# Kernel tuning notes

Hardware: AMD Instinct MI355X
Metric: run time of the kernel (lower is better)

The kernel has to match this reference:

```python
import jax, jax.numpy as jnp
import numpy as np

NH = 16          # num_attention_heads
NOPE = 128       # qk_nope_head_dim
ROPE = 64        # qk_rope_head_dim
QHD = NOPE + ROPE  # q_head_dim = 192
VD = 128         # v_head_dim
QLR = 1536       # q_lora_rank
KVLR = 512       # kv_lora_rank
HID = 2048
B, S = 1, 2048
THETA = 10000.0
EPS = 1e-6


def rms_norm(x, w, eps=EPS):
    xf = x.astype(jnp.float32)
    var = jnp.mean(xf * xf, axis=-1, keepdims=True)
    return (w * (xf * jax.lax.rsqrt(var + eps)).astype(x.dtype))


def _deinterleave(x):
    # view(..., d//2, 2).transpose(-1, -2).reshape(..., d): evens then odds
    return jnp.concatenate([x[..., 0::2], x[..., 1::2]], axis=-1)


def _rotate_half(x):
    h = x.shape[-1] // 2
    return jnp.concatenate([-x[..., h:], x[..., :h]], axis=-1)


def setup_inputs() -> dict:
    key = jax.random.key(0)
    ks = jax.random.split(key, 6)
    s = 0.02
    return {
        'hidden_states': jax.random.normal(ks[0], (B, S, HID), jnp.float32),
        'position_ids': jnp.arange(S, dtype=jnp.int32)[None, :],
        'Wqa': jax.random.normal(ks[1], (HID, QLR), jnp.float32) * s,
        'qa_ln_w': jnp.ones((QLR,), jnp.float32),
        'Wqb': jax.random.normal(ks[2], (QLR, NH * QHD), jnp.float32) * s,
        'Wkva': jax.random.normal(ks[3], (HID, KVLR + ROPE), jnp.float32) * s,
        'kv_ln_w': jnp.ones((KVLR,), jnp.float32),
        'Wkvb': jax.random.normal(ks[4], (KVLR, NH * (NOPE + VD)), jnp.float32) * s,
        'Wo': jax.random.normal(ks[5], (NH * VD, HID), jnp.float32) * s,
    }


def reference(hidden_states, position_ids, Wqa, qa_ln_w, Wqb, Wkva, kv_ln_w, Wkvb, Wo):
    b, s, _ = hidden_states.shape
    # Q path: low-rank down -> RMSNorm -> up
    q = rms_norm(hidden_states @ Wqa, qa_ln_w) @ Wqb
    q = q.reshape(b, s, NH, QHD).transpose(0, 2, 1, 3)          # (b,h,s,192)
    q_nope, q_pe = q[..., :NOPE], q[..., NOPE:]
    # KV path: compressed kv + shared rope key
    ckv = hidden_states @ Wkva                                   # (b,s,576)
    c_kv, k_pe = ckv[..., :KVLR], ckv[..., KVLR:]
    k_pe = k_pe.reshape(b, s, 1, ROPE).transpose(0, 2, 1, 3)     # (b,1,s,64)
    kv = rms_norm(c_kv, kv_ln_w) @ Wkvb
    kv = kv.reshape(b, s, NH, NOPE + VD).transpose(0, 2, 1, 3)   # (b,h,s,256)
    k_nope, v = kv[..., :NOPE], kv[..., NOPE:]
    # partial RoPE on the 64-dim rope slices
    inv_freq = 1.0 / (THETA ** (jnp.arange(0, ROPE, 2, dtype=jnp.float32) / ROPE))
    t = jnp.arange(s, dtype=jnp.float32)
    emb = jnp.concatenate([jnp.outer(t, inv_freq)] * 2, axis=-1)  # (s,64)
    cos = jnp.cos(emb)[position_ids][:, None]                     # (b,1,s,64)
    sin = jnp.sin(emb)[position_ids][:, None]
    q_pe = _deinterleave(q_pe)
    k_pe = _deinterleave(k_pe)
    q_pe = q_pe * cos + _rotate_half(q_pe) * sin
    k_pe = k_pe * cos + _rotate_half(k_pe) * sin
    query = jnp.concatenate([q_nope, q_pe], axis=-1)                       # (b,h,s,192)
    key = jnp.concatenate([k_nope, jnp.broadcast_to(k_pe, (b, NH, s, ROPE))], axis=-1)
    # causal attention, softmax_scale = q_head_dim**-0.5
    scale = QHD ** (-0.5)
    scores = jnp.einsum('bhqd,bhkd->bhqk', query, key) * scale
    mask = jnp.tril(jnp.ones((s, s), dtype=bool))
    scores = jnp.where(mask, scores, jnp.finfo(scores.dtype).min)
    probs = jax.nn.softmax(scores, axis=-1)
    attn = jnp.einsum('bhqk,bhkd->bhqd', probs, v)               # (b,h,s,128)
    out = attn.transpose(0, 2, 1, 3).reshape(b, s, NH * VD) @ Wo  # (b,s,hid)
    return out
```

## Files before the change

kernel.cpp:

```cpp
#include <hip/hip_runtime.h>
#include <hip/hip_bf16.h>

typedef unsigned short u16;
typedef _Float16 h16;
typedef h16 h16x8 __attribute__((ext_vector_type(8)));
typedef h16 h16x4 __attribute__((ext_vector_type(4)));
typedef float f32x4 __attribute__((ext_vector_type(4)));

#define S_LEN 2048
#define QLR   1536
#define KVLR  512
#define NHEAD 16
#define QHD   192
#define QHS   200
#define NOPE  128
#define VDIM  128
#define SCALE 0.07216878364870322f
#define FREQC (-0.4152410118609203f)

__device__ __forceinline__ void gld16(const h16* g, h16* l){
  __builtin_amdgcn_global_load_lds((__attribute__((address_space(1))) const void*)g,
                                   (__attribute__((address_space(3))) void*)l, 16, 0, 0);
}

__global__ __launch_bounds__(256) void k_cvt(const float* __restrict__ in, h16* __restrict__ out, int n4){
  int i = blockIdx.x * 256 + threadIdx.x;
  if (i < n4){
    float4 v = ((const float4*)in)[i];
    h16x4 o = { (h16)v.x, (h16)v.y, (h16)v.z, (h16)v.w };
    ((h16x4*)out)[i] = o;
  }
}

__global__ __launch_bounds__(256) void k_tc(const float* __restrict__ W, h16* __restrict__ WT, int K, int N){
  __shared__ float t[64][65];
  int k0 = blockIdx.y * 64, n0 = blockIdx.x * 64;
  int tid = threadIdx.x;
  int r = tid >> 4, c4 = (tid & 15) * 4;
#pragma unroll
  for (int it = 0; it < 4; it++){
    float4 v = *(const float4*)(W + (size_t)(k0 + it*16 + r) * N + n0 + c4);
    t[it*16+r][c4] = v.x; t[it*16+r][c4+1] = v.y; t[it*16+r][c4+2] = v.z; t[it*16+r][c4+3] = v.w;
  }
  __syncthreads();
  int n = tid >> 2, k16 = (tid & 3) * 16;
  h16x8 o0, o1;
#pragma unroll
  for (int e = 0; e < 8; e++){ o0[e] = (h16)t[k16 + e][n]; o1[e] = (h16)t[k16 + 8 + e][n]; }
  h16* dst = WT + (size_t)(n0 + n) * K + k0 + k16;
  *(h16x8*)dst = o0;
  *(h16x8*)(dst + 8) = o1;
}

__device__ __forceinline__ void gemm_core(const h16* __restrict__ A, const h16* __restrict__ B,
    int K, int m0, int n0, h16* As, h16* Bs, f32x4 (&acc)[4][4]){
  const int tid = threadIdx.x;
  const int lane = tid & 63, quad = lane >> 4, lr = lane & 15;
  const int wid = tid >> 6;
  const int wr = (wid >> 1) * 64, wc = (wid & 1) * 64;
  const int sr = tid >> 2, scc = (tid & 3) * 8;
  const h16* Ag = A + (size_t)(m0 + sr) * K + scc;
  const h16* Bg = B + (size_t)(n0 + sr) * K + scc;
  for (int kt = 0; kt < K; kt += 32){
    gld16(Ag + kt,                 &As[tid * 8]);
    gld16(Ag + (size_t)64*K + kt,  &As[2048 + tid * 8]);
    gld16(Bg + kt,                 &Bs[tid * 8]);
    gld16(Bg + (size_t)64*K + kt,  &Bs[2048 + tid * 8]);
    __syncthreads();
    h16x8 af[4], bfr[4];
#pragma unroll
    for (int r = 0; r < 4; r++) af[r]  = *(const h16x8*)&As[(wr + r*16 + lr) * 32 + quad * 8];
#pragma unroll
    for (int c = 0; c < 4; c++) bfr[c] = *(const h16x8*)&Bs[(wc + c*16 + lr) * 32 + quad * 8];
#pragma unroll
    for (int r = 0; r < 4; r++)
#pragma unroll
      for (int c = 0; c < 4; c++)
        acc[r][c] = __builtin_amdgcn_mfma_f32_16x16x32_f16(af[r], bfr[c], acc[r][c], 0, 0, 0);
    __syncthreads();
  }
}

template<bool OF32>
__global__ __launch_bounds__(256) void k_gemm(const h16* __restrict__ A, const h16* __restrict__ B,
                                              void* __restrict__ Cv, int N, int K){
  __shared__ __attribute__((aligned(16))) h16 As[128*32];
  __shared__ __attribute__((aligned(16))) h16 Bs[128*32];
  const int m0 = blockIdx.y * 128, n0 = blockIdx.x * 128;
  f32x4 acc[4][4] = {};
  gemm_core(A, B, K, m0, n0, As, Bs, acc);
  const int lane = threadIdx.x & 63, quad = lane >> 4, lr = lane & 15;
  const int wid = threadIdx.x >> 6;
  const int wr = (wid >> 1) * 64, wc = (wid & 1) * 64;
#pragma unroll
  for (int r = 0; r < 4; r++)
#pragma unroll
    for (int c = 0; c < 4; c++){
      int row = m0 + wr + r*16 + quad*4;
      int col = n0 + wc + c*16 + lr;
#pragma unroll
      for (int i = 0; i < 4; i++){
        float val = acc[r][c][i];
        if (OF32) ((float*)Cv)[(size_t)(row + i) * N + col] = val;
        else      ((h16*)Cv)[(size_t)(row + i) * N + col] = (h16)val;
      }
    }
}

__global__ __launch_bounds__(256) void k_norm(const h16* __restrict__ Cc,
      const float* __restrict__ qw, const float* __restrict__ kw, const int* __restrict__ pos_ids,
      h16* __restrict__ qln, h16* __restrict__ kvln, h16* __restrict__ kpe,
      float* __restrict__ cst, float* __restrict__ snt){
  const int s = blockIdx.x, tid = threadIdx.x;
  __shared__ float red[8];
  const h16* c1 = Cc + (size_t)s * 2176;
  float v[6]; float ss = 0.f;
#pragma unroll
  for (int i = 0; i < 6; i++){ v[i] = (float)c1[tid + i*256]; ss += v[i]*v[i]; }
  for (int off = 32; off > 0; off >>= 1) ss += __shfl_down(ss, off);
  if ((tid & 63) == 0) red[tid >> 6] = ss;
  __syncthreads();
  float rq = rsqrtf((red[0]+red[1]+red[2]+red[3]) / (float)QLR + 1e-6f);
#pragma unroll
  for (int i = 0; i < 6; i++)
    qln[(size_t)s * QLR + tid + i*256] = (h16)(qw[tid + i*256] * v[i] * rq);

  const h16* ck = c1 + QLR;
  float w0 = (float)ck[tid], w1 = (float)ck[tid + 256];
  float ss2 = w0*w0 + w1*w1;
  for (int off = 32; off > 0; off >>= 1) ss2 += __shfl_down(ss2, off);
  if ((tid & 63) == 0) red[4 + (tid >> 6)] = ss2;
  __syncthreads();
  float rk = rsqrtf((red[4]+red[5]+red[6]+red[7]) / (float)KVLR + 1e-6f);
  kvln[(size_t)s * KVLR + tid]       = (h16)(kw[tid] * w0 * rk);
  kvln[(size_t)s * KVLR + tid + 256] = (h16)(kw[tid + 256] * w1 * rk);

  if (tid < 32){
    int d = tid;
    float x = (float)ck[KVLR + 2*d];
    float y = (float)ck[KVLR + 2*d + 1];
    float a = (float)pos_ids[s] * exp2f(FREQC * (float)d);
    float cs = cosf(a), sn = sinf(a);
    cst[s*32 + d] = cs; snt[s*32 + d] = sn;
    kpe[(size_t)s*64 + d]      = (h16)(x*cs - y*sn);
    kpe[(size_t)s*64 + 32 + d] = (h16)(y*cs + x*sn);
  }
}

__global__ __launch_bounds__(256) void k_asm(const h16* __restrict__ Qm, const h16* __restrict__ KVm,
      const h16* __restrict__ kpe, const float* __restrict__ cst, const float* __restrict__ snt,
      h16* __restrict__ Qh, h16* __restrict__ Kh, h16* __restrict__ VT){
  const int t = blockIdx.x, h = blockIdx.y, tid = threadIdx.x;
  const int s0 = t * 64;
#pragma unroll
  for (int it = 0; it < 6; it++){
    int cid = it*256 + tid;
    int r = cid / 24, c8 = (cid - r*24) * 8;
    int rr = s0 + r;
    const h16* in = Qm + (size_t)rr*3072 + h*192;
    h16* outr = Qh + ((size_t)h*S_LEN + rr)*QHS;
    h16x8 v = *(const h16x8*)(in + c8);
    if (c8 < 128){
      h16x8 o;
#pragma unroll
      for (int e = 0; e < 8; e++) o[e] = (h16)((float)v[e] * SCALE);
      *(h16x8*)(outr + c8) = o;
    } else {
      int k4 = (c8 - 128) >> 1;
      h16x4 xo, yo;
#pragma unroll
      for (int m2 = 0; m2 < 4; m2++){
        float x = (float)v[2*m2], y = (float)v[2*m2+1];
        float cs = cst[rr*32 + k4 + m2], sn = snt[rr*32 + k4 + m2];
        xo[m2] = (h16)((x*cs - y*sn) * SCALE);
        yo[m2] = (h16)((y*cs + x*sn) * SCALE);
      }
      *(h16x4*)(outr + 128 + k4) = xo;
      *(h16x4*)(outr + 160 + k4) = yo;
    }
  }
#pragma unroll
  for (int it = 0; it < 6; it++){
    int cid = it*256 + tid;
    int r = cid / 24, c8 = (cid - r*24) * 8;
    int rr = s0 + r;
    h16* outr = Kh + ((size_t)h*S_LEN + rr)*QHS;
    if (c8 < 128){
      h16x8 v = *(const h16x8*)(KVm + (size_t)rr*4096 + h*256 + c8);
      *(h16x8*)(outr + c8) = v;
    } else {
      h16x8 v = *(const h16x8*)(kpe + (size_t)rr*64 + (c8 - 128));
      *(h16x8*)(outr + c8) = v;
    }
  }
  {
    int dv = tid >> 1, half = tid & 1;
    const h16* vin = KVm + h*256 + 128 + dv;
    h16* vout = VT + ((size_t)(h*VDIM + dv))*S_LEN + s0;
#pragma unroll
    for (int k = 0; k < 4; k++){
      h16x8 o;
#pragma unroll
      for (int e = 0; e < 8; e++)
        o[e] = vin[(size_t)(s0 + half*32 + k*8 + e) * 4096];
      *(h16x8*)(vout + ((half*32 + k*8 + 8*(dv & 7)) & 63)) = o;
    }
  }
}

__global__ __launch_bounds__(256) void k_flash(const h16* __restrict__ Qh, const h16* __restrict__ Kh,
      const h16* __restrict__ VT, h16* __restrict__ Opart, float* __restrict__ ml){
  const int tile = 31 - blockIdx.x;
  const int h = blockIdx.y;
  const int p = blockIdx.z;
  const int jlo = p * 8;
  if (jlo > tile) return;
  const int jhi = min(jlo + 8, tile + 1);
  const int m0 = tile * 64;
  __shared__ __attribute__((aligned(16))) h16 Ksm[64*QHS];
  __shared__ __attribute__((aligned(16))) h16 Vsm[144*64];
  __shared__ __attribute__((aligned(16))) h16 Psm[64*72];
  const int tid = threadIdx.x, wid = tid >> 6, lane = tid & 63, quad = lane >> 4, lr = lane & 15;

  {
    h16x4 one4 = { (h16)1.f, (h16)1.f, (h16)1.f, (h16)1.f };
    *(h16x4*)&Vsm[128*64 + tid*4] = one4;
  }

  const h16* Qg = Qh + ((size_t)h*S_LEN + m0)*QHS;
#pragma unroll
  for (int i = 0; i < 6; i++) gld16(Qg + i*2048 + tid*8, &Ksm[i*2048 + tid*8]);
  if (wid == 0) gld16(Qg + 12288 + lane*8, &Ksm[12288 + lane*8]);
  __syncthreads();
  h16x8 qf[6];
#pragma unroll
  for (int ks = 0; ks < 6; ks++)
    qf[ks] = *(const h16x8*)&Ksm[(wid*16 + lr)*QHS + ks*32 + quad*8];
  __syncthreads();

  float mst[4];
  f32x4 oacc[9] = {};
#pragma unroll
  for (int i = 0; i < 4; i++) mst[i] = -1e30f;

  for (int j = jlo; j < jhi; ++j){
    const h16* Kg = Kh + ((size_t)h*S_LEN + j*64)*QHS;
#pragma unroll
    for (int i = 0; i < 6; i++) gld16(Kg + i*2048 + tid*8, &Ksm[i*2048 + tid*8]);
    if (wid == 0) gld16(Kg + 12288 + lane*8, &Ksm[12288 + lane*8]);
    const h16* Vg = VT + (size_t)h * VDIM * S_LEN + (size_t)j * 64;
#pragma unroll
    for (int i = 0; i < 4; i++)
      gld16(Vg + (size_t)(i*32 + (tid >> 3)) * S_LEN + (tid & 7)*8, &Vsm[i*2048 + tid*8]);
    __syncthreads();

    f32x4 sc[4] = {};
#pragma unroll
    for (int ks = 0; ks < 6; ks++)
#pragma unroll
      for (int ct = 0; ct < 4; ct++){
        h16x8 kf = *(const h16x8*)&Ksm[(ct*16 + lr)*QHS + ks*32 + quad*8];
        sc[ct] = __builtin_amdgcn_mfma_f32_16x16x32_f16(qf[ks], kf, sc[ct], 0,0,0);
      }

    if (j == tile){
#pragma unroll
      for (int ct = 0; ct < 4; ct++)
#pragma unroll
        for (int i = 0; i < 4; i++)
          if (ct*16 + lr > wid*16 + quad*4 + i) sc[ct][i] = -1e30f;
    }

    float al[4];
#pragma unroll
    for (int i = 0; i < 4; i++){
      float m = fmaxf(fmaxf(sc[0][i], sc[1][i]), fmaxf(sc[2][i], sc[3][i]));
#pragma unroll
      for (int off = 1; off < 16; off <<= 1) m = fmaxf(m, __shfl_xor(m, off));
      float mn = fmaxf(mst[i], m);
      al[i] = __expf(mst[i] - mn);
      mst[i] = mn;
    }
#pragma unroll
    for (int ct = 0; ct < 4; ct++)
#pragma unroll
      for (int i = 0; i < 4; i++)
        Psm[(wid*16 + quad*4 + i)*72 + ct*16 + lr] = (h16)__expf(sc[ct][i] - mst[i]);
#pragma unroll
    for (int oc = 0; oc < 9; oc++)
#pragma unroll
      for (int i = 0; i < 4; i++) oacc[oc][i] *= al[i];

#pragma unroll
    for (int ks2 = 0; ks2 < 2; ks2++){
      h16x8 pf = *(const h16x8*)&Psm[(wid*16 + lr)*72 + ks2*32 + quad*8];
#pragma unroll
      for (int oc = 0; oc < 9; oc++){
        int cv = (ks2*32 + quad*8 + 8*(lr & 7)) & 63;
        h16x8 vf = *(const h16x8*)&Vsm[(oc*16 + lr)*64 + cv];
        oacc[oc] = __builtin_amdgcn_mfma_f32_16x16x32_f16(pf, vf, oacc[oc], 0,0,0);
      }
    }
    __syncthreads();
  }

  const int part = (tile*NHEAD + h)*4 + p;
  h16* Op = Opart + (size_t)part * 8192;
#pragma unroll
  for (int oc = 0; oc < 8; oc++)
#pragma unroll
    for (int i = 0; i < 4; i++)
      Op[(wid*16 + quad*4 + i)*128 + oc*16 + lr] = (h16)oacc[oc][i];
  if (lr == 0){
#pragma unroll
    for (int i = 0; i < 4; i++){
      int r = wid*16 + quad*4 + i;
      ml[(size_t)part*128 + r*2]     = mst[i];
      ml[(size_t)part*128 + r*2 + 1] = oacc[8][i];
    }
  }
}

__global__ __launch_bounds__(256) void k_comb(const h16* __restrict__ Opart, const float* __restrict__ ml,
                                              h16* __restrict__ Ob){
  const int t = blockIdx.x, h = blockIdx.y, tid = threadIdx.x;
  const int P = t/8 + 1;
  const int r = tid >> 2, c0 = (tid & 3) * 32;
  const int base = (t*NHEAD + h)*4;
  float w[4]; float M = -1e30f, denom = 0.f;
  for (int p = 0; p < P; p++) M = fmaxf(M, ml[(size_t)(base+p)*128 + r*2]);
  for (int p = 0; p < P; p++){
    w[p] = __expf(ml[(size_t)(base+p)*128 + r*2] - M);
    denom += w[p] * ml[(size_t)(base+p)*128 + r*2 + 1];
  }
  float inv = 1.f / denom;
#pragma unroll
  for (int ch = 0; ch < 4; ch++){
    float a[8] = {};
    for (int p = 0; p < P; p++){
      h16x8 v = *(const h16x8*)&Opart[(size_t)(base+p)*8192 + r*128 + c0 + ch*8];
#pragma unroll
      for (int e = 0; e < 8; e++) a[e] += w[p] * (float)v[e];
    }
    h16x8 o;
#pragma unroll
    for (int e = 0; e < 8; e++) o[e] = (h16)(a[e] * inv);
    *(h16x8*)&Ob[((size_t)(t*64 + r))*(NHEAD*VDIM) + h*VDIM + c0 + ch*8] = o;
  }
}

extern "C" void kernel_launch(void* const* d_in, const int* in_sizes, int n_in,
                              void* d_out, int out_size, void* d_ws, size_t ws_size,
                              hipStream_t stream){
  const float* hidden = (const float*)d_in[0];
  const int*   pos    = (const int*)  d_in[1];
  const float* Wqa    = (const float*)d_in[2];
  const float* qaw    = (const float*)d_in[3];
  const float* Wqb    = (const float*)d_in[4];
  const float* Wkva   = (const float*)d_in[5];
  const float* kvw    = (const float*)d_in[6];
  const float* Wkvb   = (const float*)d_in[7];
  const float* Wo     = (const float*)d_in[8];

  h16* ws = (h16*)d_ws;
  size_t off = 0;
  auto take = [&](size_t n){ h16* p = ws + off; off += n; return p; };
  h16* hb    = take(2048ull * 2048);
  h16* Wc    = take(2176ull * 2048);
  h16* WqbT  = take(3072ull * 1536);
  h16* WkvbT = take(4096ull * 512);
  h16* WoT   = take(2048ull * 2048);
  h16* Ccomb = take(2048ull * 2176);
  h16* qln   = take(2048ull * 1536);
  h16* kvln  = take(2048ull * 512);
  h16* kpe   = take(2048ull * 64);
  float* cst = (float*)take(2048ull * 64);
  float* snt = (float*)take(2048ull * 64);
  h16* Qm    = take(2048ull * 3072);
  h16* KVm   = take(2048ull * 4096);
  h16* Qh    = take(16ull * 2048 * QHS);
  h16* Kh    = take(16ull * 2048 * QHS);
  h16* VT    = take(16ull * 128 * 2048);
  h16* Ob    = hb;
  h16*   Opart = qln;
  float* mlbuf = (float*)Wc;

  k_cvt<<<4096, 256, 0, stream>>>(hidden, hb, 1048576);
  k_tc<<<dim3(24, 32), 256, 0, stream>>>(Wqa,  Wc,                 2048, 1536);
  k_tc<<<dim3( 9, 32), 256, 0, stream>>>(Wkva, Wc + 1536ull*2048,  2048, 576);
  k_tc<<<dim3(48, 24), 256, 0, stream>>>(Wqb,  WqbT,  1536, 3072);
  k_tc<<<dim3(64,  8), 256, 0, stream>>>(Wkvb, WkvbT, 512,  4096);
  k_tc<<<dim3(32, 32), 256, 0, stream>>>(Wo,   WoT,   2048, 2048);

  k_gemm<false><<<dim3(17, 16), 256, 0, stream>>>(hb, Wc, Ccomb, 2176, 2048);
  k_norm<<<2048, 256, 0, stream>>>(Ccomb, qaw, kvw, pos, qln, kvln, kpe, cst, snt);
  k_gemm<false><<<dim3(24, 16), 256, 0, stream>>>(qln,  WqbT,  Qm,  3072, 1536);
  k_gemm<false><<<dim3(32, 16), 256, 0, stream>>>(kvln, WkvbT, KVm, 4096, 512);
  k_asm<<<dim3(32, 16), 256, 0, stream>>>(Qm, KVm, kpe, cst, snt, Qh, Kh, VT);
  k_flash<<<dim3(32, 16, 4), 256, 0, stream>>>(Qh, Kh, VT, Opart, mlbuf);
  k_comb<<<dim3(32, 16), 256, 0, stream>>>(Opart, mlbuf, Ob);
  k_gemm<true><<<dim3(16, 16), 256, 0, stream>>>(Ob, WoT, d_out, 2048, 2048);
}
```

Baseline: 398.6 us.

## Fuse head assembly into Q/KV GEMM epilogues and double flash query tile

Removes the separate k_asm pass. Q-up GEMM now writes scaled, RoPE-rotated Q straight into the per-head padded layout, KV-up GEMM writes K-nope and transposed V (via an LDS transpose), and k_norm broadcasts the rotated k_pe into Kh. This drops the Qm/KVm intermediates and an extra read-write pass over them. The flash kernel now processes 128 query rows per block (two 16-row tiles per wave, sharing each K/V tile load), with k_comb adjusted to match. The cost is strided scalar epilogue stores, more registers in flash, and fewer flash blocks.

```diff
diff --git a/kernel.cpp b/kernel.cpp
--- a/kernel.cpp
+++ b/kernel.cpp
@@ -13,7 +13,6 @@
 #define NHEAD 16
 #define QHD   192
 #define QHS   200
-#define NOPE  128
 #define VDIM  128
 #define SCALE 0.07216878364870322f
 #define FREQC (-0.4152410118609203f)
@@ -107,12 +106,101 @@
     }
 }
 
+__global__ __launch_bounds__(256) void k_gemm_q(const h16* __restrict__ A, const h16* __restrict__ B,
+      h16* __restrict__ Qh, const float* __restrict__ cst, const float* __restrict__ snt){
+  __shared__ __attribute__((aligned(16))) h16 As[128*32];
+  __shared__ __attribute__((aligned(16))) h16 Bs[128*32];
+  const int m0 = blockIdx.y * 128, n0 = blockIdx.x * 128;
+  f32x4 acc[4][4] = {};
+  gemm_core(A, B, QLR, m0, n0, As, Bs, acc);
+  const int lane = threadIdx.x & 63, quad = lane >> 4, lr = lane & 15;
+  const int wid = threadIdx.x >> 6;
+  const int wr = (wid >> 1) * 64, wc = (wid & 1) * 64;
+#pragma unroll
+  for (int r = 0; r < 4; r++)
+#pragma unroll
+    for (int c = 0; c < 4; c++){
+      int row0 = m0 + wr + r*16 + quad*4;
+      int cg = n0 + wc + c*16 + lr;
+      int head = cg / 192;
+      int inner = cg - head*192;
+      h16* outb = Qh + ((size_t)head*S_LEN)*QHS;
+      if (inner < 128){
+#pragma unroll
+        for (int i = 0; i < 4; i++)
+          outb[(size_t)(row0+i)*QHS + inner] = (h16)(acc[r][c][i] * SCALE);
+      } else {
+        int d = (inner - 128) >> 1;
+        int isY = inner & 1;
+        int ocol = (isY ? 160 : 128) + d;
+#pragma unroll
+        for (int i = 0; i < 4; i++){
+          int rr = row0 + i;
+          float cs = cst[rr*32 + d], sn = snt[rr*32 + d];
+          float v = acc[r][c][i];
+          float w = __shfl_xor(v, 1);
+          float out = isY ? (v*cs + w*sn) : (v*cs - w*sn);
+          outb[(size_t)rr*QHS + ocol] = (h16)(out * SCALE);
+        }
+      }
+    }
+}
+
+__global__ __launch_bounds__(256) void k_gemm_kv(const h16* __restrict__ A, const h16* __restrict__ B,
+      h16* __restrict__ Kh, h16* __restrict__ VT){
+  __shared__ __attribute__((aligned(16))) h16 As[128*32];
+  __shared__ __attribute__((aligned(16))) h16 Bs[128*32];
+  __shared__ __attribute__((aligned(16))) h16 tsm[128*132];
+  const int m0 = blockIdx.y * 128, n0 = blockIdx.x * 128;
+  f32x4 acc[4][4] = {};
+  gemm_core(A, B, KVLR, m0, n0, As, Bs, acc);
+  const int tid = threadIdx.x;
+  const int lane = tid & 63, quad = lane >> 4, lr = lane & 15;
+  const int wid = tid >> 6;
+  const int wr = (wid >> 1) * 64, wc = (wid & 1) * 64;
+  const int head = n0 >> 8;
+  if ((n0 & 128) == 0){
+#pragma unroll
+    for (int r = 0; r < 4; r++)
+#pragma unroll
+      for (int c = 0; c < 4; c++){
+        int row0 = m0 + wr + r*16 + quad*4;
+        int inner = wc + c*16 + lr;
+#pragma unroll
+        for (int i = 0; i < 4; i++)
+          Kh[((size_t)head*S_LEN + row0 + i)*QHS + inner] = (h16)acc[r][c][i];
+      }
+  } else {
+#pragma unroll
+    for (int r = 0; r < 4; r++)
+#pragma unroll
+      for (int c = 0; c < 4; c++){
+        int lrow = wr + r*16 + quad*4;
+        int dv = wc + c*16 + lr;
+#pragma unroll
+        for (int i = 0; i < 4; i++)
+          tsm[(lrow + i)*132 + dv] = (h16)acc[r][c][i];
+      }
+    __syncthreads();
+    int dv = tid >> 1, sh = (tid & 1) * 64;
+    h16* vout = VT + ((size_t)(head*VDIM + dv))*S_LEN + m0 + sh;
+#pragma unroll
+    for (int ko = 0; ko < 8; ko++){
+      h16x8 o;
+#pragma unroll
+      for (int e = 0; e < 8; e++) o[e] = tsm[(sh + ko*8 + e)*132 + dv];
+      *(h16x8*)(vout + ((ko*8 + 8*(dv & 7)) & 63)) = o;
+    }
+  }
+}
+
 __global__ __launch_bounds__(256) void k_norm(const h16* __restrict__ Cc,
       const float* __restrict__ qw, const float* __restrict__ kw, const int* __restrict__ pos_ids,
-      h16* __restrict__ qln, h16* __restrict__ kvln, h16* __restrict__ kpe,
+      h16* __restrict__ qln, h16* __restrict__ kvln, h16* __restrict__ Kh,
       float* __restrict__ cst, float* __restrict__ snt){
   const int s = blockIdx.x, tid = threadIdx.x;
   __shared__ float red[8];
+  __shared__ h16 kpe_s[64];
   const h16* c1 = Cc + (size_t)s * 2176;
   float v[6]; float ss = 0.f;
 #pragma unroll
@@ -142,84 +230,30 @@
     float a = (float)pos_ids[s] * exp2f(FREQC * (float)d);
     float cs = cosf(a), sn = sinf(a);
     cst[s*32 + d] = cs; snt[s*32 + d] = sn;
-    kpe[(size_t)s*64 + d]      = (h16)(x*cs - y*sn);
-    kpe[(size_t)s*64 + 32 + d] = (h16)(y*cs + x*sn);
-  }
-}
-
-__global__ __launch_bounds__(256) void k_asm(const h16* __restrict__ Qm, const h16* __restrict__ KVm,
-      const h16* __restrict__ kpe, const float* __restrict__ cst, const float* __restrict__ snt,
-      h16* __restrict__ Qh, h16* __restrict__ Kh, h16* __restrict__ VT){
-  const int t = blockIdx.x, h = blockIdx.y, tid = threadIdx.x;
-  const int s0 = t * 64;
-#pragma unroll
-  for (int it = 0; it < 6; it++){
-    int cid = it*256 + tid;
-    int r = cid / 24, c8 = (cid - r*24) * 8;
-    int rr = s0 + r;
-    const h16* in = Qm + (size_t)rr*3072 + h*192;
-    h16* outr = Qh + ((size_t)h*S_LEN + rr)*QHS;
-    h16x8 v = *(const h16x8*)(in + c8);
-    if (c8 < 128){
-      h16x8 o;
-#pragma unroll
-      for (int e = 0; e < 8; e++) o[e] = (h16)((float)v[e] * SCALE);
-      *(h16x8*)(outr + c8) = o;
-    } else {
-      int k4 = (c8 - 128) >> 1;
-      h16x4 xo, yo;
-#pragma unroll
-      for (int m2 = 0; m2 < 4; m2++){
-        float x = (float)v[2*m2], y = (float)v[2*m2+1];
-        float cs = cst[rr*32 + k4 + m2], sn = snt[rr*32 + k4 + m2];
-        xo[m2] = (h16)((x*cs - y*sn) * SCALE);
-        yo[m2] = (h16)((y*cs + x*sn) * SCALE);
-      }
-      *(h16x4*)(outr + 128 + k4) = xo;
-      *(h16x4*)(outr + 160 + k4) = yo;
-    }
-  }
-#pragma unroll
-  for (int it = 0; it < 6; it++){
-    int cid = it*256 + tid;
-    int r = cid / 24, c8 = (cid - r*24) * 8;
-    int rr = s0 + r;
-    h16* outr = Kh + ((size_t)h*S_LEN + rr)*QHS;
-    if (c8 < 128){
-      h16x8 v = *(const h16x8*)(KVm + (size_t)rr*4096 + h*256 + c8);
-      *(h16x8*)(outr + c8) = v;
-    } else {
-      h16x8 v = *(const h16x8*)(kpe + (size_t)rr*64 + (c8 - 128));
-      *(h16x8*)(outr + c8) = v;
-    }
-  }
+    kpe_s[d]      = (h16)(x*cs - y*sn);
+    kpe_s[32 + d] = (h16)(y*cs + x*sn);
+  }
+  __syncthreads();
   {
-    int dv = tid >> 1, half = tid & 1;
-    const h16* vin = KVm + h*256 + 128 + dv;
-    h16* vout = VT + ((size_t)(h*VDIM + dv))*S_LEN + s0;
-#pragma unroll
-    for (int k = 0; k < 4; k++){
-      h16x8 o;
-#pragma unroll
-      for (int e = 0; e < 8; e++)
-        o[e] = vin[(size_t)(s0 + half*32 + k*8 + e) * 4096];
-      *(h16x8*)(vout + ((half*32 + k*8 + 8*(dv & 7)) & 63)) = o;
-    }
-  }
-}
-
-__global__ __launch_bounds__(256) void k_flash(const h16* __restrict__ Qh, const h16* __restrict__ Kh,
+    int h = tid >> 4, seg = (tid & 15) * 4;
+    h16x4 o = { kpe_s[seg], kpe_s[seg+1], kpe_s[seg+2], kpe_s[seg+3] };
+    *(h16x4*)&Kh[((size_t)h*S_LEN + s)*QHS + 128 + seg] = o;
+  }
+}
+
+__global__ __launch_bounds__(256, 2) void k_flash(const h16* __restrict__ Qh, const h16* __restrict__ Kh,
       const h16* __restrict__ VT, h16* __restrict__ Opart, float* __restrict__ ml){
-  const int tile = 31 - blockIdx.x;
+  const int tile = 15 - blockIdx.x;
   const int h = blockIdx.y;
   const int p = blockIdx.z;
+  const int jcount = 2*tile + 2;
   const int jlo = p * 8;
-  if (jlo > tile) return;
-  const int jhi = min(jlo + 8, tile + 1);
-  const int m0 = tile * 64;
+  if (jlo >= jcount) return;
+  const int jhi = min(jlo + 8, jcount);
+  const int m0 = tile * 128;
   __shared__ __attribute__((aligned(16))) h16 Ksm[64*QHS];
   __shared__ __attribute__((aligned(16))) h16 Vsm[144*64];
-  __shared__ __attribute__((aligned(16))) h16 Psm[64*72];
+  __shared__ __attribute__((aligned(16))) h16 Psm[128*72];
   const int tid = threadIdx.x, wid = tid >> 6, lane = tid & 63, quad = lane >> 4, lr = lane & 15;
 
   {
@@ -227,96 +261,108 @@
     *(h16x4*)&Vsm[128*64 + tid*4] = one4;
   }
 
-  const h16* Qg = Qh + ((size_t)h*S_LEN + m0)*QHS;
-#pragma unroll
-  for (int i = 0; i < 6; i++) gld16(Qg + i*2048 + tid*8, &Ksm[i*2048 + tid*8]);
-  if (wid == 0) gld16(Qg + 12288 + lane*8, &Ksm[12288 + lane*8]);
-  __syncthreads();
-  h16x8 qf[6];
-#pragma unroll
-  for (int ks = 0; ks < 6; ks++)
-    qf[ks] = *(const h16x8*)&Ksm[(wid*16 + lr)*QHS + ks*32 + quad*8];
-  __syncthreads();
-
-  float mst[4];
-  f32x4 oacc[9] = {};
-#pragma unroll
-  for (int i = 0; i < 4; i++) mst[i] = -1e30f;
+  const h16* Qbase = Qh + ((size_t)h*S_LEN + m0)*QHS;
+  h16x8 qf[2][6];
+#pragma unroll
+  for (int rt = 0; rt < 2; rt++)
+#pragma unroll
+    for (int ks = 0; ks < 6; ks++)
+      qf[rt][ks] = *(const h16x8*)(Qbase + (size_t)(wid*32 + rt*16 + lr)*QHS + ks*32 + quad*8);
+
+  float mst[2][4];
+  f32x4 oacc[2][9] = {};
+#pragma unroll
+  for (int rt = 0; rt < 2; rt++)
+#pragma unroll
+    for (int i = 0; i < 4; i++) mst[rt][i] = -1e30f;
 
   for (int j = jlo; j < jhi; ++j){
     const h16* Kg = Kh + ((size_t)h*S_LEN + j*64)*QHS;
 #pragma unroll
     for (int i = 0; i < 6; i++) gld16(Kg + i*2048 + tid*8, &Ksm[i*2048 + tid*8]);
-    if (wid == 0) gld16(Kg + 12288 + lane*8, &Ksm[12288 + lane*8]);
+    if (tid < 64) gld16(Kg + 12288 + tid*8, &Ksm[12288 + tid*8]);
     const h16* Vg = VT + (size_t)h * VDIM * S_LEN + (size_t)j * 64;
 #pragma unroll
     for (int i = 0; i < 4; i++)
       gld16(Vg + (size_t)(i*32 + (tid >> 3)) * S_LEN + (tid & 7)*8, &Vsm[i*2048 + tid*8]);
     __syncthreads();
 
-    f32x4 sc[4] = {};
+    f32x4 sc[2][4] = {};
 #pragma unroll
     for (int ks = 0; ks < 6; ks++)
 #pragma unroll
       for (int ct = 0; ct < 4; ct++){
         h16x8 kf = *(const h16x8*)&Ksm[(ct*16 + lr)*QHS + ks*32 + quad*8];
-        sc[ct] = __builtin_amdgcn_mfma_f32_16x16x32_f16(qf[ks], kf, sc[ct], 0,0,0);
-      }
-
-    if (j == tile){
+        sc[0][ct] = __builtin_amdgcn_mfma_f32_16x16x32_f16(qf[0][ks], kf, sc[0][ct], 0,0,0);
+        sc[1][ct] = __builtin_amdgcn_mfma_f32_16x16x32_f16(qf[1][ks], kf, sc[1][ct], 0,0,0);
+      }
+
+    if (j >= 2*tile){
+#pragma unroll
+      for (int rt = 0; rt < 2; rt++)
+#pragma unroll
+        for (int ct = 0; ct < 4; ct++){
+          int kcol = j*64 + ct*16 + lr;
+#pragma unroll
+          for (int i = 0; i < 4; i++)
+            if (kcol > m0 + wid*32 + rt*16 + quad*4 + i) sc[rt][ct][i] = -1e30f;
+        }
+    }
+
+#pragma unroll
+    for (int rt = 0; rt < 2; rt++){
+      float al[4];
+#pragma unroll
+      for (int i = 0; i < 4; i++){
+        float m = fmaxf(fmaxf(sc[rt][0][i], sc[rt][1][i]), fmaxf(sc[rt][2][i], sc[rt][3][i]));
+#pragma unroll
+        for (int off = 1; off < 16; off <<= 1) m = fmaxf(m, __shfl_xor(m, off));
+        float mn = fmaxf(fmaxf(mst[rt][i], m), -1e29f);
+        al[i] = __expf(mst[rt][i] - mn);
+        mst[rt][i] = mn;
+      }
 #pragma unroll
       for (int ct = 0; ct < 4; ct++)
 #pragma unroll
         for (int i = 0; i < 4; i++)
-          if (ct*16 + lr > wid*16 + quad*4 + i) sc[ct][i] = -1e30f;
-    }
-
-    float al[4];
-#pragma unroll
-    for (int i = 0; i < 4; i++){
-      float m = fmaxf(fmaxf(sc[0][i], sc[1][i]), fmaxf(sc[2][i], sc[3][i]));
-#pragma unroll
-      for (int off = 1; off < 16; off <<= 1) m = fmaxf(m, __shfl_xor(m, off));
-      float mn = fmaxf(mst[i], m);
-      al[i] = __expf(mst[i] - mn);
-      mst[i] = mn;
-    }
-#pragma unroll
-    for (int ct = 0; ct < 4; ct++)
+          Psm[(wid*32 + rt*16 + quad*4 + i)*72 + ct*16 + lr] = (h16)__expf(sc[rt][ct][i] - mst[rt][i]);
+#pragma unroll
+      for (int oc = 0; oc < 9; oc++)
+#pragma unroll
+        for (int i = 0; i < 4; i++) oacc[rt][oc][i] *= al[i];
+    }
+
+#pragma unroll
+    for (int ks2 = 0; ks2 < 2; ks2++){
+      h16x8 pf0 = *(const h16x8*)&Psm[(wid*32 + lr)*72      + ks2*32 + quad*8];
+      h16x8 pf1 = *(const h16x8*)&Psm[(wid*32 + 16 + lr)*72 + ks2*32 + quad*8];
+      int cv = (ks2*32 + quad*8 + 8*(lr & 7)) & 63;
+#pragma unroll
+      for (int oc = 0; oc < 9; oc++){
+        h16x8 vf = *(const h16x8*)&Vsm[(oc*16 + lr)*64 + cv];
+        oacc[0][oc] = __builtin_amdgcn_mfma_f32_16x16x32_f16(pf0, vf, oacc[0][oc], 0,0,0);
+        oacc[1][oc] = __builtin_amdgcn_mfma_f32_16x16x32_f16(pf1, vf, oacc[1][oc], 0,0,0);
+      }
+    }
+    __syncthreads();
+  }
+
+  const int part = (tile*NHEAD + h)*4 + p;
+  h16* Op = Opart + (size_t)part * 16384;
+#pragma unroll
+  for (int rt = 0; rt < 2; rt++){
+#pragma unroll
+    for (int oc = 0; oc < 8; oc++)
 #pragma unroll
       for (int i = 0; i < 4; i++)
-        Psm[(wid*16 + quad*4 + i)*72 + ct*16 + lr] = (h16)__expf(sc[ct][i] - mst[i]);
-#pragma unroll
-    for (int oc = 0; oc < 9; oc++)
-#pragma unroll
-      for (int i = 0; i < 4; i++) oacc[oc][i] *= al[i];
-
-#pragma unroll
-    for (int ks2 = 0; ks2 < 2; ks2++){
-      h16x8 pf = *(const h16x8*)&Psm[(wid*16 + lr)*72 + ks2*32 + quad*8];
-#pragma unroll
-      for (int oc = 0; oc < 9; oc++){
-        int cv = (ks2*32 + quad*8 + 8*(lr & 7)) & 63;
-        h16x8 vf = *(const h16x8*)&Vsm[(oc*16 + lr)*64 + cv];
-        oacc[oc] = __builtin_amdgcn_mfma_f32_16x16x32_f16(pf, vf, oacc[oc], 0,0,0);
-      }
-    }
-    __syncthreads();
-  }
-
-  const int part = (tile*NHEAD + h)*4 + p;
-  h16* Op = Opart + (size_t)part * 8192;
-#pragma unroll
-  for (int oc = 0; oc < 8; oc++)
-#pragma unroll
-    for (int i = 0; i < 4; i++)
-      Op[(wid*16 + quad*4 + i)*128 + oc*16 + lr] = (h16)oacc[oc][i];
-  if (lr == 0){
-#pragma unroll
-    for (int i = 0; i < 4; i++){
-      int r = wid*16 + quad*4 + i;
-      ml[(size_t)part*128 + r*2]     = mst[i];
-      ml[(size_t)part*128 + r*2 + 1] = oacc[8][i];
+        Op[(wid*32 + rt*16 + quad*4 + i)*128 + oc*16 + lr] = (h16)oacc[rt][oc][i];
+    if (lr == 0){
+#pragma unroll
+      for (int i = 0; i < 4; i++){
+        int r = wid*32 + rt*16 + quad*4 + i;
+        ml[(size_t)part*256 + r*2]     = mst[rt][i];
+        ml[(size_t)part*256 + r*2 + 1] = oacc[rt][8][i];
+      }
     }
   }
 }
@@ -324,28 +370,28 @@
 __global__ __launch_bounds__(256) void k_comb(const h16* __restrict__ Opart, const float* __restrict__ ml,
                                               h16* __restrict__ Ob){
   const int t = blockIdx.x, h = blockIdx.y, tid = threadIdx.x;
-  const int P = t/8 + 1;
-  const int r = tid >> 2, c0 = (tid & 3) * 32;
+  const int P = (2*t + 9) >> 3;
+  const int r = tid >> 1, c0 = (tid & 1) * 64;
   const int base = (t*NHEAD + h)*4;
   float w[4]; float M = -1e30f, denom = 0.f;
-  for (int p = 0; p < P; p++) M = fmaxf(M, ml[(size_t)(base+p)*128 + r*2]);
+  for (int p = 0; p < P; p++) M = fmaxf(M, ml[(size_t)(base+p)*256 + r*2]);
   for (int p = 0; p < P; p++){
-    w[p] = __expf(ml[(size_t)(base+p)*128 + r*2] - M);
-    denom += w[p] * ml[(size_t)(base+p)*128 + r*2 + 1];
+    w[p] = __expf(ml[(size_t)(base+p)*256 + r*2] - M);
+    denom += w[p] * ml[(size_t)(base+p)*256 + r*2 + 1];
   }
   float inv = 1.f / denom;
 #pragma unroll
-  for (int ch = 0; ch < 4; ch++){
+  for (int ch = 0; ch < 8; ch++){
     float a[8] = {};
     for (int p = 0; p < P; p++){
-      h16x8 v = *(const h16x8*)&Opart[(size_t)(base+p)*8192 + r*128 + c0 + ch*8];
+      h16x8 v = *(const h16x8*)&Opart[(size_t)(base+p)*16384 + r*128 + c0 + ch*8];
 #pragma unroll
       for (int e = 0; e < 8; e++) a[e] += w[p] * (float)v[e];
     }
     h16x8 o;
 #pragma unroll
     for (int e = 0; e < 8; e++) o[e] = (h16)(a[e] * inv);
-    *(h16x8*)&Ob[((size_t)(t*64 + r))*(NHEAD*VDIM) + h*VDIM + c0 + ch*8] = o;
+    *(h16x8*)&Ob[((size_t)(t*128 + r))*(NHEAD*VDIM) + h*VDIM + c0 + ch*8] = o;
   }
 }
 
@@ -366,24 +412,21 @@
   size_t off = 0;
   auto take = [&](size_t n){ h16* p = ws + off; off += n; return p; };
   h16* hb    = take(2048ull * 2048);
+  h16* WoT   = take(2048ull * 2048);
   h16* Wc    = take(2176ull * 2048);
   h16* WqbT  = take(3072ull * 1536);
   h16* WkvbT = take(4096ull * 512);
-  h16* WoT   = take(2048ull * 2048);
   h16* Ccomb = take(2048ull * 2176);
   h16* qln   = take(2048ull * 1536);
   h16* kvln  = take(2048ull * 512);
-  h16* kpe   = take(2048ull * 64);
   float* cst = (float*)take(2048ull * 64);
   float* snt = (float*)take(2048ull * 64);
-  h16* Qm    = take(2048ull * 3072);
-  h16* KVm   = take(2048ull * 4096);
   h16* Qh    = take(16ull * 2048 * QHS);
   h16* Kh    = take(16ull * 2048 * QHS);
   h16* VT    = take(16ull * 128 * 2048);
   h16* Ob    = hb;
-  h16*   Opart = qln;
-  float* mlbuf = (float*)Wc;
+  h16*   Opart = Wc;
+  float* mlbuf = (float*)(Wc + 16ull*16*4*16384);
 
   k_cvt<<<4096, 256, 0, stream>>>(hidden, hb, 1048576);
   k_tc<<<dim3(24, 32), 256, 0, stream>>>(Wqa,  Wc,                 2048, 1536);
@@ -393,11 +436,10 @@
   k_tc<<<dim3(32, 32), 256, 0, stream>>>(Wo,   WoT,   2048, 2048);
 
   k_gemm<false><<<dim3(17, 16), 256, 0, stream>>>(hb, Wc, Ccomb, 2176, 2048);
-  k_norm<<<2048, 256, 0, stream>>>(Ccomb, qaw, kvw, pos, qln, kvln, kpe, cst, snt);
-  k_gemm<false><<<dim3(24, 16), 256, 0, stream>>>(qln,  WqbT,  Qm,  3072, 1536);
-  k_gemm<false><<<dim3(32, 16), 256, 0, stream>>>(kvln, WkvbT, KVm, 4096, 512);
-  k_asm<<<dim3(32, 16), 256, 0, stream>>>(Qm, KVm, kpe, cst, snt, Qh, Kh, VT);
-  k_flash<<<dim3(32, 16, 4), 256, 0, stream>>>(Qh, Kh, VT, Opart, mlbuf);
-  k_comb<<<dim3(32, 16), 256, 0, stream>>>(Opart, mlbuf, Ob);
+  k_norm<<<2048, 256, 0, stream>>>(Ccomb, qaw, kvw, pos, qln, kvln, Kh, cst, snt);
+  k_gemm_q <<<dim3(24, 16), 256, 0, stream>>>(qln,  WqbT,  Qh, cst, snt);
+  k_gemm_kv<<<dim3(32, 16), 256, 0, stream>>>(kvln, WkvbT, Kh, VT);
+  k_flash<<<dim3(16, 16, 4), 256, 0, stream>>>(Qh, Kh, VT, Opart, mlbuf);
+  k_comb<<<dim3(16, 16), 256, 0, stream>>>(Opart, mlbuf, Ob);
   k_gemm<true><<<dim3(16, 16), 256, 0, stream>>>(Ob, WoT, d_out, 2048, 2048);
 }
```

Result: faster. 383.6 us (-3.8%).
